# Kernel tuning notes

Hardware: AMD Instinct MI355X
Metric: run time of the kernel (lower is better)

The kernel has to match this reference:

```python
import jax, jax.numpy as jnp
import numpy as np

B, C, T = 8, 128, 32768
OUT, K, DIL = 128, 2, 2


def dilated_indices(T, k, d):
    # Faithful vectorized version of the original Python double loop:
    # idx[span*k + j] = span + j*d, clamped to T (the zero-pad slot) when >= T+1.
    padded = T + 1
    idx = jnp.arange(padded)[:, None] + jnp.arange(k)[None, :] * d  # (padded, k)
    idx = idx.reshape(-1)                                           # (k*padded,)
    return jnp.where(idx >= padded, T, idx)


def setup_inputs() -> dict:
    key = jax.random.key(0)
    k1, k2, k3 = jax.random.split(key, 3)
    x = jax.random.normal(k1, (B, C, T), dtype=jnp.float32)
    # Conv1d(in=C, out=OUT, kernel_size=K) parameters
    W = jax.random.normal(k2, (OUT, C, K), dtype=jnp.float32) * 0.05
    b = jax.random.normal(k3, (OUT,), dtype=jnp.float32) * 0.05
    return {"x": x, "W": W, "b": b}


def reference(x, W, b):
    Bx, Cx, Tx = x.shape
    # pad one zero column at the end of the time axis (torch.cat with zeros)
    xp = jnp.concatenate([x, jnp.zeros((Bx, Cx, 1), x.dtype)], axis=2)  # (B,C,T+1)
    idx = dilated_indices(Tx, K, DIL)                                   # (K*(T+1),)
    swizzle = xp[:, :, idx]                                             # (B,C,K*(T+1))
    # Conv1d with stride == kernel_size over the swizzled buffer is a GEMM
    # over non-overlapping windows of size K.
    sw = swizzle.reshape(Bx, Cx, Tx + 1, K)                             # (B,C,T+1,K)
    out = jnp.einsum('bcpk,ock->bop', sw, W) + b[None, :, None]         # (B,OUT,T+1)
    return out
```

## Files before the change

kernel.cpp:

```cpp
#include <hip/hip_runtime.h>


namespace {

constexpr int kB   = 8;
constexpr int kC   = 128;
constexpr int kT   = 32768;
constexpr int kP   = kT + 1;
constexpr int kOut = 128;
constexpr int kNP  = 128;
constexpr int kNTiles = (kP + kNP - 1) / kNP;
constexpr int kLStride = 136;

typedef __attribute__((ext_vector_type(8))) short short8;
typedef __attribute__((ext_vector_type(4))) float f32x4;

__device__ __forceinline__ short f2bf(float f) {
    unsigned int u = __builtin_bit_cast(unsigned int, f);
    u += 0x7fffu + ((u >> 16) & 1u);
    return (short)(u >> 16);
}

template <bool GUARD>
__device__ __forceinline__ void stage_tile(const float* __restrict__ xb,
                                           short* __restrict__ xs,
                                           int tid, int p0) {
    {
        const int pos = tid & 127;
        const int gp  = p0 + pos;
        const bool ok = !GUARD || (gp < kT);
        const float* col = xb + (ok ? gp : 0);
        const int c0base = (tid >> 7) * 64;
        #pragma unroll
        for (int ch = 0; ch < 8; ++ch) {
            const int c0 = c0base + ch * 8;
            float r[8];
            #pragma unroll
            for (int j = 0; j < 8; ++j) r[j] = col[(c0 + j) << 15];
            short8 v;
            #pragma unroll
            for (int j = 0; j < 8; ++j) v[j] = ok ? f2bf(r[j]) : (short)0;
            *reinterpret_cast<short8*>(xs + pos * kLStride + c0) = v;
        }
    }
    if (tid < 32) {
        const int pos = 128 + (tid & 1);
        const int gp  = p0 + pos;
        const bool ok = !GUARD || (gp < kT);
        const float* col = xb + (ok ? gp : 0);
        const int c0 = (tid >> 1) * 8;
        float r[8];
        #pragma unroll
        for (int j = 0; j < 8; ++j) r[j] = col[(c0 + j) << 15];
        short8 v;
        #pragma unroll
        for (int j = 0; j < 8; ++j) v[j] = ok ? f2bf(r[j]) : (short)0;
        *reinterpret_cast<short8*>(xs + pos * kLStride + c0) = v;
    }
}

__global__ __launch_bounds__(256, 2) void dconv_mfma(
    const float* __restrict__ x, const float* __restrict__ W,
    const float* __restrict__ bias, float* __restrict__ out)
{
    __shared__ __align__(16) short xs[130 * kLStride];

    const int tid  = threadIdx.x;
    const int lane = tid & 63;
    const int wv   = tid >> 6;
    const int bb   = blockIdx.x / kNTiles;
    const int tile = blockIdx.x % kNTiles;
    const int p0   = tile * kNP;

    const int rowbase = wv * 32;
    short8 wf[2][2][4];
    #pragma unroll
    for (int cc = 0; cc < 2; ++cc) {
        const int o = rowbase + cc * 16 + (lane & 15);
        #pragma unroll
        for (int s = 0; s < 4; ++s) {
            const int cb = s * 32 + (lane >> 4) * 8;
            const float4* wp = reinterpret_cast<const float4*>(W + o * (kC * 2) + cb * 2);
            float4 wr[4];
            #pragma unroll
            for (int q = 0; q < 4; ++q) wr[q] = wp[q];
            short8 f0, f1;
            #pragma unroll
            for (int q = 0; q < 4; ++q) {
                f0[q * 2 + 0] = f2bf(wr[q].x);  f1[q * 2 + 0] = f2bf(wr[q].y);
                f0[q * 2 + 1] = f2bf(wr[q].z);  f1[q * 2 + 1] = f2bf(wr[q].w);
            }
            wf[0][cc][s] = f0;
            wf[1][cc][s] = f1;
        }
    }

    const float* xb = x + (size_t)bb * kC * kT;
    if (p0 + 129 < kT) stage_tile<false>(xb, xs, tid, p0);
    else               stage_tile<true>(xb, xs, tid, p0);

    f32x4 acc[2][8];
    #pragma unroll
    for (int cc = 0; cc < 2; ++cc) {
        const int ob = rowbase + cc * 16 + (lane >> 4) * 4;
        f32x4 a;
        a[0] = bias[ob + 0]; a[1] = bias[ob + 1];
        a[2] = bias[ob + 2]; a[3] = bias[ob + 3];
        #pragma unroll
        for (int nc = 0; nc < 8; ++nc) acc[cc][nc] = a;
    }

    __syncthreads();

    #pragma unroll
    for (int tap = 0; tap < 2; ++tap) {
        #pragma unroll
        for (int s = 0; s < 4; ++s) {
            const int cb = s * 32 + (lane >> 4) * 8;
            #pragma unroll
            for (int nc = 0; nc < 8; ++nc) {
                const int pos = nc * 16 + (lane & 15) + 2 * tap;
                const short8 bf = *reinterpret_cast<const short8*>(xs + pos * kLStride + cb);
                acc[0][nc] = __builtin_amdgcn_mfma_f32_16x16x32_bf16(wf[tap][0][s], bf, acc[0][nc], 0, 0, 0);
                acc[1][nc] = __builtin_amdgcn_mfma_f32_16x16x32_bf16(wf[tap][1][s], bf, acc[1][nc], 0, 0, 0);
            }
        }
    }

    float* ob = out + (size_t)bb * kOut * kP;
    #pragma unroll
    for (int nc = 0; nc < 8; ++nc) {
        const int col = p0 + nc * 16 + (lane & 15);
        if (col < kP) {
            #pragma unroll
            for (int cc = 0; cc < 2; ++cc) {
                const int orow = rowbase + cc * 16 + (lane >> 4) * 4;
                #pragma unroll
                for (int r = 0; r < 4; ++r) {
                    ob[(size_t)(orow + r) * kP + col] = acc[cc][nc][r];
                }
            }
        }
    }
}

}

extern "C" void kernel_launch(void* const* d_in, const int* in_sizes, int n_in,
                              void* d_out, int out_size, void* d_ws, size_t ws_size,
                              hipStream_t stream) {
    const float* x    = (const float*)d_in[0];
    const float* W    = (const float*)d_in[1];
    const float* bias = (const float*)d_in[2];
    float* out        = (float*)d_out;

    dim3 grid(kB * kNTiles);
    dim3 block(256);
    hipLaunchKernelGGL(dconv_mfma, grid, block, 0, stream, x, W, bias, out);
}
```

Baseline: 279.9 us.

## Make blocks persistent over four tiles with double-buffered LDS and swapped MFMA operands

Each block now processes four consecutive 128-position tiles. The next tile's global loads are issued into registers and written to a second LDS buffer while the current tile is computed and stored, which overlaps memory with compute. The staging loads become float4-vectorised, the LDS layout gains an XOR swizzle to reduce bank conflicts, and the MFMA operands are swapped so each lane writes four contiguous outputs as a float4. The final padded output column is filled with the bias by the first eight blocks. The cost is more registers and LDS per block and fewer blocks in flight, and output stores are unaligned because kP is odd.

```diff
diff --git a/kernel.cpp b/kernel.cpp
--- a/kernel.cpp
+++ b/kernel.cpp
@@ -3,14 +3,16 @@
 
 namespace {
 
-constexpr int kB   = 8;
 constexpr int kC   = 128;
 constexpr int kT   = 32768;
 constexpr int kP   = kT + 1;
 constexpr int kOut = 128;
 constexpr int kNP  = 128;
-constexpr int kNTiles = (kP + kNP - 1) / kNP;
+constexpr int kTilesPerB = kT / kNP;
+constexpr int kUnitsPerBlock = 4;
+constexpr int kNBlocks = 512;
 constexpr int kLStride = 136;
+constexpr int kLBuf    = 130 * kLStride;
 
 typedef __attribute__((ext_vector_type(8))) short short8;
 typedef __attribute__((ext_vector_type(4))) float f32x4;
@@ -21,41 +23,61 @@
     return (short)(u >> 16);
 }
 
-template <bool GUARD>
-__device__ __forceinline__ void stage_tile(const float* __restrict__ xb,
-                                           short* __restrict__ xs,
-                                           int tid, int p0) {
-    {
-        const int pos = tid & 127;
-        const int gp  = p0 + pos;
-        const bool ok = !GUARD || (gp < kT);
-        const float* col = xb + (ok ? gp : 0);
-        const int c0base = (tid >> 7) * 64;
-        #pragma unroll
-        for (int ch = 0; ch < 8; ++ch) {
-            const int c0 = c0base + ch * 8;
-            float r[8];
-            #pragma unroll
-            for (int j = 0; j < 8; ++j) r[j] = col[(c0 + j) << 15];
+__device__ __forceinline__ int lds_idx(int pos, int c) {
+    return pos * kLStride + (c ^ (((pos >> 2) & 7) << 3));
+}
+
+__device__ __forceinline__ void lds_barrier() {
+    asm volatile("s_waitcnt lgkmcnt(0)" ::: "memory");
+    __builtin_amdgcn_s_barrier();
+}
+
+struct StageRegs {
+    f32x4 m[16];
+    float h[8];
+};
+
+__device__ __forceinline__ void stage_issue(const float* __restrict__ xb, int p0,
+                                            int tid, StageRegs& r) {
+    const int pgrp = tid & 31;
+    const int cgrp = tid >> 5;
+    const float* col = xb + p0 + pgrp * 4;
+    #pragma unroll
+    for (int j = 0; j < 16; ++j) {
+        r.m[j] = *reinterpret_cast<const f32x4*>(col + ((size_t)(cgrp * 16 + j) << 15));
+    }
+    if (tid < 32) {
+        const int gph = p0 + 128 + (tid & 1);
+        const float* colh = xb + (gph < kT ? gph : 0);
+        const int c0 = (tid >> 1) * 8;
+        #pragma unroll
+        for (int j = 0; j < 8; ++j) r.h[j] = colh[(size_t)(c0 + j) << 15];
+    }
+}
+
+__device__ __forceinline__ void stage_commit(short* __restrict__ xs, int p0,
+                                             int tid, const StageRegs& r) {
+    const int pgrp = tid & 31;
+    const int cgrp = tid >> 5;
+    #pragma unroll
+    for (int i = 0; i < 4; ++i) {
+        const int pos = pgrp * 4 + i;
+        #pragma unroll
+        for (int h = 0; h < 2; ++h) {
             short8 v;
             #pragma unroll
-            for (int j = 0; j < 8; ++j) v[j] = ok ? f2bf(r[j]) : (short)0;
-            *reinterpret_cast<short8*>(xs + pos * kLStride + c0) = v;
+            for (int j = 0; j < 8; ++j) v[j] = f2bf(r.m[h * 8 + j][i]);
+            *reinterpret_cast<short8*>(xs + lds_idx(pos, cgrp * 16 + h * 8)) = v;
         }
     }
     if (tid < 32) {
         const int pos = 128 + (tid & 1);
-        const int gp  = p0 + pos;
-        const bool ok = !GUARD || (gp < kT);
-        const float* col = xb + (ok ? gp : 0);
+        const bool okh = (p0 + pos) < kT;
         const int c0 = (tid >> 1) * 8;
-        float r[8];
-        #pragma unroll
-        for (int j = 0; j < 8; ++j) r[j] = col[(c0 + j) << 15];
         short8 v;
         #pragma unroll
-        for (int j = 0; j < 8; ++j) v[j] = ok ? f2bf(r[j]) : (short)0;
-        *reinterpret_cast<short8*>(xs + pos * kLStride + c0) = v;
+        for (int j = 0; j < 8; ++j) v[j] = okh ? f2bf(r.h[j]) : (short)0;
+        *reinterpret_cast<short8*>(xs + lds_idx(pos, c0)) = v;
     }
 }
 
@@ -63,14 +85,19 @@
     const float* __restrict__ x, const float* __restrict__ W,
     const float* __restrict__ bias, float* __restrict__ out)
 {
-    __shared__ __align__(16) short xs[130 * kLStride];
+    __shared__ __align__(16) short xs[2][kLBuf];
 
     const int tid  = threadIdx.x;
     const int lane = tid & 63;
     const int wv   = tid >> 6;
-    const int bb   = blockIdx.x / kNTiles;
-    const int tile = blockIdx.x % kNTiles;
-    const int p0   = tile * kNP;
+    const int blk  = blockIdx.x;
+    const int u0   = blk * kUnitsPerBlock;
+    const int bb   = u0 >> 8;
+    const int t0   = u0 & 255;
+
+    if (blk < 8 && tid < kOut) {
+        out[(size_t)blk * kOut * kP + (size_t)tid * kP + kT] = bias[tid];
+    }
 
     const int rowbase = wv * 32;
     short8 wf[2][2][4];
@@ -80,67 +107,81 @@
         #pragma unroll
         for (int s = 0; s < 4; ++s) {
             const int cb = s * 32 + (lane >> 4) * 8;
-            const float4* wp = reinterpret_cast<const float4*>(W + o * (kC * 2) + cb * 2);
-            float4 wr[4];
+            const f32x4* wp = reinterpret_cast<const f32x4*>(W + o * (kC * 2) + cb * 2);
+            f32x4 wr[4];
             #pragma unroll
             for (int q = 0; q < 4; ++q) wr[q] = wp[q];
             short8 f0, f1;
             #pragma unroll
             for (int q = 0; q < 4; ++q) {
-                f0[q * 2 + 0] = f2bf(wr[q].x);  f1[q * 2 + 0] = f2bf(wr[q].y);
-                f0[q * 2 + 1] = f2bf(wr[q].z);  f1[q * 2 + 1] = f2bf(wr[q].w);
+                f0[q * 2 + 0] = f2bf(wr[q][0]);  f1[q * 2 + 0] = f2bf(wr[q][1]);
+                f0[q * 2 + 1] = f2bf(wr[q][2]);  f1[q * 2 + 1] = f2bf(wr[q][3]);
             }
             wf[0][cc][s] = f0;
             wf[1][cc][s] = f1;
         }
     }
+    const float bv0 = bias[rowbase + (lane & 15)];
+    const float bv1 = bias[rowbase + 16 + (lane & 15)];
 
     const float* xb = x + (size_t)bb * kC * kT;
-    if (p0 + 129 < kT) stage_tile<false>(xb, xs, tid, p0);
-    else               stage_tile<true>(xb, xs, tid, p0);
-
-    f32x4 acc[2][8];
-    #pragma unroll
-    for (int cc = 0; cc < 2; ++cc) {
-        const int ob = rowbase + cc * 16 + (lane >> 4) * 4;
-        f32x4 a;
-        a[0] = bias[ob + 0]; a[1] = bias[ob + 1];
-        a[2] = bias[ob + 2]; a[3] = bias[ob + 3];
-        #pragma unroll
-        for (int nc = 0; nc < 8; ++nc) acc[cc][nc] = a;
-    }
-
-    __syncthreads();
-
-    #pragma unroll
-    for (int tap = 0; tap < 2; ++tap) {
-        #pragma unroll
-        for (int s = 0; s < 4; ++s) {
-            const int cb = s * 32 + (lane >> 4) * 8;
-            #pragma unroll
-            for (int nc = 0; nc < 8; ++nc) {
-                const int pos = nc * 16 + (lane & 15) + 2 * tap;
-                const short8 bf = *reinterpret_cast<const short8*>(xs + pos * kLStride + cb);
-                acc[0][nc] = __builtin_amdgcn_mfma_f32_16x16x32_bf16(wf[tap][0][s], bf, acc[0][nc], 0, 0, 0);
-                acc[1][nc] = __builtin_amdgcn_mfma_f32_16x16x32_bf16(wf[tap][1][s], bf, acc[1][nc], 0, 0, 0);
-            }
-        }
-    }
-
     float* ob = out + (size_t)bb * kOut * kP;
-    #pragma unroll
-    for (int nc = 0; nc < 8; ++nc) {
-        const int col = p0 + nc * 16 + (lane & 15);
-        if (col < kP) {
-            #pragma unroll
-            for (int cc = 0; cc < 2; ++cc) {
-                const int orow = rowbase + cc * 16 + (lane >> 4) * 4;
+
+    StageRegs r;
+    stage_issue(xb, t0 << 7, tid, r);
+    stage_commit(xs[0], t0 << 7, tid, r);
+    stage_issue(xb, (t0 + 1) << 7, tid, r);
+    lds_barrier();
+
+    #pragma unroll 1
+    for (int i = 0; i < kUnitsPerBlock; ++i) {
+        const short* cur = xs[i & 1];
+        const int p0 = (t0 + i) << 7;
+
+        f32x4 acc[2][8];
+        #pragma unroll
+        for (int nc = 0; nc < 8; ++nc) {
+            #pragma unroll
+            for (int rr = 0; rr < 4; ++rr) { acc[0][nc][rr] = bv0; acc[1][nc][rr] = bv1; }
+        }
+        #pragma unroll
+        for (int tap = 0; tap < 2; ++tap) {
+            #pragma unroll
+            for (int s = 0; s < 4; ++s) {
+                const int cb = s * 32 + (lane >> 4) * 8;
                 #pragma unroll
-                for (int r = 0; r < 4; ++r) {
-                    ob[(size_t)(orow + r) * kP + col] = acc[cc][nc][r];
+                for (int nc = 0; nc < 8; ++nc) {
+                    const int pos = nc * 16 + (lane & 15) + 2 * tap;
+                    const short8 xf = *reinterpret_cast<const short8*>(cur + lds_idx(pos, cb));
+                    acc[0][nc] = __builtin_amdgcn_mfma_f32_16x16x32_bf16(xf, wf[tap][0][s], acc[0][nc], 0, 0, 0);
+                    acc[1][nc] = __builtin_amdgcn_mfma_f32_16x16x32_bf16(xf, wf[tap][1][s], acc[1][nc], 0, 0, 0);
                 }
             }
         }
+
+        if (i + 1 < kUnitsPerBlock) {
+            stage_commit(xs[(i + 1) & 1], (t0 + i + 1) << 7, tid, r);
+        }
+
+        {
+            const int o0   = rowbase + (lane & 15);
+            const int prow = (lane >> 4) * 4;
+            #pragma unroll
+            for (int nc = 0; nc < 8; ++nc) {
+                const int p = p0 + nc * 16 + prow;
+                #pragma unroll
+                for (int cc = 0; cc < 2; ++cc) {
+                    __builtin_memcpy(ob + (size_t)(o0 + cc * 16) * kP + p, &acc[cc][nc],
+                                     sizeof(f32x4));
+                }
+            }
+        }
+
+        if (i + 2 < kUnitsPerBlock) {
+            stage_issue(xb, (t0 + i + 2) << 7, tid, r);
+        }
+
+        if (i + 1 < kUnitsPerBlock) lds_barrier();
     }
 }
 
@@ -154,7 +195,7 @@
     const float* bias = (const float*)d_in[2];
     float* out        = (float*)d_out;
 
-    dim3 grid(kB * kNTiles);
+    dim3 grid(kNBlocks);
     dim3 block(256);
     hipLaunchKernelGGL(dconv_mfma, grid, block, 0, stream, x, W, bias, out);
 }
```

New measurement: 305.6 us. 9.2% more time.
